# Performance work log

Measured on AMD Instinct MI355X. Metric: run time of the kernel, lower is better.

## Reference

```python
import jax, jax.numpy as jnp
import numpy as np


def setup_inputs() -> dict:
    key = jax.random.key(0)
    k1, k2 = jax.random.split(key)
    # x: [B, C_in, H, W]
    x = jax.random.normal(k1, (32, 256, 56, 56), dtype=jnp.float32)
    # weight: [C_out, C_in, kH, kW]; weight_init_std ~ small-std gaussian init
    weight = jax.random.normal(k2, (512, 256, 3, 3), dtype=jnp.float32) * 0.02
    return {"x": x, "weight": weight}


def reference(x, weight):
    # HebbianConv2d default inference path: out_sim = kernel_mult2d (plain conv2d,
    # stride 1, VALID padding), out_act = identity, out_bias=False, out_cmp=False,
    # weight_zeta_mode=None so get_weight() == weight.
    y = jax.lax.conv_general_dilated(
        x, weight,
        window_strides=(1, 1),
        padding="VALID",
        dimension_numbers=("NCHW", "OIHW", "NCHW"),
    )  # [B, C_out, H-kH+1, W-kW+1] = [32, 512, 54, 54]
    return y
```

## Files before the change

kernel.cpp:

```cpp
#include <hip/hip_runtime.h>

typedef __attribute__((ext_vector_type(8))) short short8;
typedef __attribute__((ext_vector_type(4))) float f32x4;

#define B_    32
#define CI_   256
#define H_    56
#define HW_   3136
#define CO_   512
#define OHW_  54
#define PIXB_ 2916
#define NPIX_ 93312

#define XT_BYTES 51380224ull
#define WS_NEED  53739520ull

__device__ __forceinline__ ushort f2bf(float f) {
  unsigned u = __float_as_uint(f);
  unsigned r = (u + 0x7FFFu + ((u >> 16) & 1u)) >> 16;
  return (ushort)r;
}

__device__ __forceinline__ void async16(const void* g, void* l) {
  __builtin_amdgcn_global_load_lds(
      (const __attribute__((address_space(1))) unsigned int*)g,
      (__attribute__((address_space(3))) unsigned int*)l, 16, 0, 0);
}

__global__ void transpose_x(const float* __restrict__ x, ushort* __restrict__ xt) {
  __shared__ float tile[64][65];
  const int b   = blockIdx.z;
  const int hw0 = blockIdx.x * 64;
  const int ci0 = blockIdx.y * 64;
  const int t = threadIdx.x;
  const int hwl = t & 63, cil = t >> 6;
  const float* xp = x + ((size_t)b * CI_ + ci0) * HW_ + hw0;
  #pragma unroll
  for (int i = 0; i < 16; ++i) {
    int ci = i * 4 + cil;
    tile[ci][hwl] = xp[(size_t)ci * HW_ + hwl];
  }
  __syncthreads();
  const int cil2 = t & 63, hwl2 = t >> 6;
  ushort* op = xt + ((size_t)b * HW_ + hw0) * CI_ + ci0;
  #pragma unroll
  for (int i = 0; i < 16; ++i) {
    int hw = i * 4 + hwl2;
    op[(size_t)hw * CI_ + cil2] = f2bf(tile[cil2][hw]);
  }
}

__global__ void repack_w(const float* __restrict__ w, ushort* __restrict__ wt) {
  const int co = blockIdx.x, khkw = blockIdx.y, ci = threadIdx.x;
  float v = w[((size_t)co * CI_ + ci) * 9 + khkw];
  wt[((size_t)khkw * CO_ + co) * CI_ + ci] = f2bf(v);
}

__global__ __launch_bounds__(256, 3)
void conv_mfma(const ushort* __restrict__ xt, const ushort* __restrict__ wt,
               float* __restrict__ out) {
  __shared__ ushort lds_w[128 * 32];
  __shared__ ushort lds_x[128 * 32];

  const int t    = threadIdx.x;
  const int lane = t & 63;
  const int wv   = t >> 6;
  const int quad = lane >> 4;
  const int l16  = lane & 15;
  const int P0   = blockIdx.x * 128;
  const int co0  = blockIdx.y * 128;

  const int row0 = wv * 32 + (lane >> 2);
  const int ci8  = (lane & 3) * 8;

  const size_t wA0 = (size_t)(co0 + row0) * CI_ + ci8;
  const size_t wA1 = (size_t)(co0 + row0 + 16) * CI_ + ci8;

  int P_a = P0 + row0;
  int b_a = P_a / PIXB_; int rem_a = P_a - b_a * PIXB_;
  int oh_a = rem_a / OHW_; int ow_a = rem_a - oh_a * OHW_;
  const size_t xB0 = ((size_t)b_a * HW_ + oh_a * H_ + ow_a) * CI_ + ci8;
  int P_b = P_a + 16;
  int b_b = P_b / PIXB_; int rem_b = P_b - b_b * PIXB_;
  int oh_b = rem_b / OHW_; int ow_b = rem_b - oh_b * OHW_;
  const size_t xB1 = ((size_t)b_b * HW_ + oh_b * H_ + ow_b) * CI_ + ci8;

  char* ldsw_c = (char*)lds_w + wv * 2048;
  char* ldsx_c = (char*)lds_x + wv * 2048;

  f32x4 acc[4][4];
  #pragma unroll
  for (int i = 0; i < 4; ++i)
    #pragma unroll
    for (int j = 0; j < 4; ++j) acc[i][j] = (f32x4){0.f, 0.f, 0.f, 0.f};

  const int wm = (wv & 1) * 64;
  const int wn = (wv >> 1) * 64;

  for (int khkw = 0; khkw < 9; ++khkw) {
    const int kh = khkw / 3, kw = khkw - kh * 3;
    const size_t w_off = (size_t)khkw * CO_ * CI_;
    const size_t x_off = (size_t)(kh * H_ + kw) * CI_;
    for (int ci0 = 0; ci0 < CI_; ci0 += 32) {
      async16(wt + wA0 + w_off + ci0, ldsw_c);
      async16(wt + wA1 + w_off + ci0, ldsw_c + 1024);
      async16(xt + xB0 + x_off + ci0, ldsx_c);
      async16(xt + xB1 + x_off + ci0, ldsx_c + 1024);
      __syncthreads();

      short8 af[4], bfr[4];
      #pragma unroll
      for (int mt = 0; mt < 4; ++mt)
        af[mt] = *(const short8*)&lds_w[(wm + mt * 16 + l16) * 32 + quad * 8];
      #pragma unroll
      for (int nt = 0; nt < 4; ++nt)
        bfr[nt] = *(const short8*)&lds_x[(wn + nt * 16 + l16) * 32 + quad * 8];
      #pragma unroll
      for (int mt = 0; mt < 4; ++mt)
        #pragma unroll
        for (int nt = 0; nt < 4; ++nt)
          acc[mt][nt] = __builtin_amdgcn_mfma_f32_16x16x32_bf16(
              af[mt], bfr[nt], acc[mt][nt], 0, 0, 0);

      __syncthreads();
    }
  }

  #pragma unroll
  for (int nt = 0; nt < 4; ++nt) {
    int P = P0 + wn + nt * 16 + l16;
    int b = P / PIXB_; int rem = P - b * PIXB_;
    size_t obase = (size_t)b * (CO_ * PIXB_) + rem;
    #pragma unroll
    for (int mt = 0; mt < 4; ++mt) {
      int cobase = co0 + wm + mt * 16 + quad * 4;
      #pragma unroll
      for (int r = 0; r < 4; ++r)
        out[obase + (size_t)(cobase + r) * PIXB_] = acc[mt][nt][r];
    }
  }
}

__global__ void naive_conv(const float* __restrict__ x, const float* __restrict__ w,
                           float* __restrict__ out) {
  size_t i = (size_t)blockIdx.x * 256 + threadIdx.x;
  if (i >= (size_t)NPIX_ * CO_ / 1) { }
  if (i >= (size_t)47775744ull) return;
  int ow = (int)(i % OHW_); size_t r = i / OHW_;
  int oh = (int)(r % OHW_); r /= OHW_;
  int co = (int)(r % CO_);  int b = (int)(r / CO_);
  const float* xp = x + (size_t)b * CI_ * HW_;
  const float* wp = w + (size_t)co * CI_ * 9;
  float acc = 0.f;
  for (int ci = 0; ci < CI_; ++ci) {
    const float* xr = xp + (size_t)ci * HW_ + oh * H_ + ow;
    const float* wr = wp + ci * 9;
    #pragma unroll
    for (int kh = 0; kh < 3; ++kh)
      #pragma unroll
      for (int kw = 0; kw < 3; ++kw)
        acc += xr[kh * H_ + kw] * wr[kh * 3 + kw];
  }
  out[i] = acc;
}

extern "C" void kernel_launch(void* const* d_in, const int* in_sizes, int n_in,
                              void* d_out, int out_size, void* d_ws, size_t ws_size,
                              hipStream_t stream) {
  const float* x = (const float*)d_in[0];
  const float* w = (const float*)d_in[1];
  float* out = (float*)d_out;

  if (ws_size >= WS_NEED) {
    ushort* xt = (ushort*)d_ws;
    ushort* wt = (ushort*)((char*)d_ws + XT_BYTES);
    transpose_x<<<dim3(49, 4, 32), 256, 0, stream>>>(x, xt);
    repack_w<<<dim3(512, 9), 256, 0, stream>>>(w, wt);
    conv_mfma<<<dim3(729, 4), 256, 0, stream>>>(xt, wt, out);
  } else {
    naive_conv<<<(47775744 + 255) / 256, 256, 0, stream>>>(x, w, out);
  }
}
```

Measured before the change: 559.4 us.

## Vectorize input transpose, coalesce weight repack, and reorder conv block mapping

The input transpose now has each block cover all 256 channels for 64 pixels. It uses float4 global loads, converts to bf16 into a padded LDS tile, then writes full 16-byte rows of the NHWC bf16 output. The weight repack stages each output channel's 2304 floats in LDS so both reads and writes are coalesced, replacing a strided gather. The conv grid is flattened so the four output-channel tiles sharing one pixel tile launch adjacently, which should improve L2 reuse of the input tile; the cost is extra integer work and higher LDS use in the transpose.

```diff
diff --git a/kernel.cpp b/kernel.cpp
--- a/kernel.cpp
+++ b/kernel.cpp
@@ -27,33 +27,59 @@
       (__attribute__((address_space(3))) unsigned int*)l, 16, 0, 0);
 }
 
-__global__ void transpose_x(const float* __restrict__ x, ushort* __restrict__ xt) {
-  __shared__ float tile[64][65];
-  const int b   = blockIdx.z;
-  const int hw0 = blockIdx.x * 64;
-  const int ci0 = blockIdx.y * 64;
+#define CIP 260
+__global__ __launch_bounds__(256)
+void transpose_x(const float* __restrict__ x, ushort* __restrict__ xt) {
+  __shared__ ushort tile[64 * CIP];
+  const int b = blockIdx.y, hw0 = blockIdx.x * 64;
   const int t = threadIdx.x;
-  const int hwl = t & 63, cil = t >> 6;
-  const float* xp = x + ((size_t)b * CI_ + ci0) * HW_ + hw0;
-  #pragma unroll
-  for (int i = 0; i < 16; ++i) {
-    int ci = i * 4 + cil;
-    tile[ci][hwl] = xp[(size_t)ci * HW_ + hwl];
+  const int j = t & 15, q = t >> 4;
+  const int hw4 = j * 4;
+  const float* xb = x + (size_t)b * CI_ * HW_ + hw0;
+
+  #pragma unroll
+  for (int p = 0; p < 4; ++p) {
+    const int c0 = p * 64 + q * 4;
+    float4 v[4];
+    #pragma unroll
+    for (int r = 0; r < 4; ++r)
+      v[r] = *(const float4*)(xb + (size_t)(c0 + r) * HW_ + hw4);
+    #pragma unroll
+    for (int r2 = 0; r2 < 4; ++r2) {
+      ushort4 o;
+      o.x = f2bf(((const float*)&v[0])[r2]);
+      o.y = f2bf(((const float*)&v[1])[r2]);
+      o.z = f2bf(((const float*)&v[2])[r2]);
+      o.w = f2bf(((const float*)&v[3])[r2]);
+      *(ushort4*)&tile[(hw4 + r2) * CIP + c0] = o;
+    }
   }
   __syncthreads();
-  const int cil2 = t & 63, hwl2 = t >> 6;
-  ushort* op = xt + ((size_t)b * HW_ + hw0) * CI_ + ci0;
-  #pragma unroll
-  for (int i = 0; i < 16; ++i) {
-    int hw = i * 4 + hwl2;
-    op[(size_t)hw * CI_ + cil2] = f2bf(tile[cil2][hw]);
-  }
-}
-
-__global__ void repack_w(const float* __restrict__ w, ushort* __restrict__ wt) {
-  const int co = blockIdx.x, khkw = blockIdx.y, ci = threadIdx.x;
-  float v = w[((size_t)co * CI_ + ci) * 9 + khkw];
-  wt[((size_t)khkw * CO_ + co) * CI_ + ci] = f2bf(v);
+
+  ushort* ob = xt + ((size_t)b * HW_ + hw0) * CI_;
+  #pragma unroll
+  for (int p = 0; p < 8; ++p) {
+    const int hw  = p * 8 + (t >> 5);
+    const int ci8 = (t & 31) * 8;
+    const ushort* src = &tile[hw * CIP + ci8];
+    uint2 lo = *(const uint2*)src;
+    uint2 hi = *(const uint2*)(src + 4);
+    uint4 v; v.x = lo.x; v.y = lo.y; v.z = hi.x; v.w = hi.y;
+    *(uint4*)(ob + (size_t)hw * CI_ + ci8) = v;
+  }
+}
+
+__global__ __launch_bounds__(256)
+void repack_w(const float* __restrict__ w, ushort* __restrict__ wt) {
+  __shared__ float buf[2304];
+  const int co = blockIdx.x, t = threadIdx.x;
+  const float* wp = w + (size_t)co * 2304;
+  #pragma unroll
+  for (int p = 0; p < 9; ++p) buf[p * 256 + t] = wp[p * 256 + t];
+  __syncthreads();
+  #pragma unroll
+  for (int k = 0; k < 9; ++k)
+    wt[(size_t)k * CO_ * CI_ + (size_t)co * CI_ + t] = f2bf(buf[t * 9 + k]);
 }
 
 __global__ __launch_bounds__(256, 3)
@@ -67,8 +93,8 @@
   const int wv   = t >> 6;
   const int quad = lane >> 4;
   const int l16  = lane & 15;
-  const int P0   = blockIdx.x * 128;
-  const int co0  = blockIdx.y * 128;
+  const int co0  = (blockIdx.x & 3) * 128;
+  const int P0   = (blockIdx.x >> 2) * 128;
 
   const int row0 = wv * 32 + (lane >> 2);
   const int ci8  = (lane & 3) * 8;
@@ -144,7 +170,6 @@
 __global__ void naive_conv(const float* __restrict__ x, const float* __restrict__ w,
                            float* __restrict__ out) {
   size_t i = (size_t)blockIdx.x * 256 + threadIdx.x;
-  if (i >= (size_t)NPIX_ * CO_ / 1) { }
   if (i >= (size_t)47775744ull) return;
   int ow = (int)(i % OHW_); size_t r = i / OHW_;
   int oh = (int)(r % OHW_); r /= OHW_;
@@ -174,9 +199,9 @@
   if (ws_size >= WS_NEED) {
     ushort* xt = (ushort*)d_ws;
     ushort* wt = (ushort*)((char*)d_ws + XT_BYTES);
-    transpose_x<<<dim3(49, 4, 32), 256, 0, stream>>>(x, xt);
-    repack_w<<<dim3(512, 9), 256, 0, stream>>>(w, wt);
-    conv_mfma<<<dim3(729, 4), 256, 0, stream>>>(xt, wt, out);
+    transpose_x<<<dim3(49, 32), 256, 0, stream>>>(x, xt);
+    repack_w<<<dim3(512), 256, 0, stream>>>(w, wt);
+    conv_mfma<<<dim3(2916), 256, 0, stream>>>(xt, wt, out);
   } else {
     naive_conv<<<(47775744 + 255) / 256, 256, 0, stream>>>(x, w, out);
   }
```

Result: no change. 556.4 us (-0.5%).
